# Kernel optimization log

Measured on AMD Instinct MI355X. Metric: run time of the kernel, lower is better.

## Reference

```python
import jax, jax.numpy as jnp
import numpy as np

B, S, D_MODEL, N_HEAD, D_HEAD, GROUPS = 2, 1024, 768, 12, 64, 4
EPS = 1e-9
SCALE = 1.0 / np.sqrt(D_HEAD).astype(np.float32)


def grouped_proj(x, W, b=None):
    # grouped 1x1 Conv1d == block-diagonal linear. x: [B,S,D], W: [g, D/g, O/g]
    g = W.shape[0]
    b_, s_, d = x.shape
    y = jnp.einsum("bsgi,gio->bsgo", x.reshape(b_, s_, g, d // g), W).reshape(b_, s_, -1)
    return y if b is None else y + b


def rel_shift_gather(pos_attn, context_len, shift):
    # HF Funnel _relative_shift_gather
    b, n, s, m = pos_attn.shape
    pos_attn = pos_attn.reshape(b, n, m, s)[:, :, shift:, :]
    pos_attn = pos_attn.reshape(b, n, s, m - shift)[..., :context_len]
    return pos_attn


def setup_inputs() -> dict:
    key = jax.random.key(0)
    ks = jax.random.split(key, 16)
    dg = D_MODEL // GROUPS          # in-channels per group
    og = (N_HEAD * D_HEAD) // GROUPS  # out-channels per group
    std = 0.02
    return {
        "query": jax.random.normal(ks[0], (B, S, D_MODEL), jnp.float32),
        "position_embeds": jax.random.normal(ks[1], (2 * S - 1, D_MODEL), jnp.float32),
        "Wq": jax.random.normal(ks[2], (GROUPS, dg, og), jnp.float32) * std,
        "Wk": jax.random.normal(ks[3], (GROUPS, dg, og), jnp.float32) * std,
        "bk": jnp.zeros((N_HEAD * D_HEAD,), jnp.float32),
        "Wv": jax.random.normal(ks[4], (GROUPS, dg, dg), jnp.float32) * std,
        "bv": jnp.zeros((D_MODEL,), jnp.float32),
        "r_kernel": jax.random.normal(ks[5], (D_MODEL, N_HEAD, D_HEAD), jnp.float32) * std,
        "r_w_bias": jax.random.normal(ks[6], (N_HEAD, D_HEAD), jnp.float32) * std,
        "r_r_bias": jax.random.normal(ks[7], (N_HEAD, D_HEAD), jnp.float32) * std,
        "Wo": jax.random.normal(ks[8], (D_MODEL, D_MODEL), jnp.float32) * std,
        "bo": jnp.zeros((D_MODEL,), jnp.float32),
        "gamma": jnp.ones((D_MODEL,), jnp.float32),
        "beta": jnp.zeros((D_MODEL,), jnp.float32),
    }


def reference(query, position_embeds, Wq, Wk, bk, Wv, bv, r_kernel, r_w_bias,
              r_r_bias, Wo, bo, gamma, beta):
    b, s, _ = query.shape
    # q/k/v via grouped 1x1 convs
    q = grouped_proj(query, Wq).reshape(b, s, N_HEAD, D_HEAD) * SCALE
    k = grouped_proj(query, Wk, bk).reshape(b, s, N_HEAD, D_HEAD)
    v = grouped_proj(query, Wv, bv).reshape(b, s, N_HEAD, D_MODEL // N_HEAD)
    # content stream: (q + u) k^T
    content_score = jnp.einsum("bind,bjnd->bnij", q + r_w_bias * SCALE, k)
    # position stream: (q + v) r^T over 2S-1 relative positions, then rel-shift
    r_head = jnp.einsum("td,dnh->tnh", position_embeds, r_kernel)
    pos_score = jnp.einsum("bind,tnd->bnit", q + r_r_bias * SCALE, r_head)
    pos_score = rel_shift_gather(pos_score, s, shift=1)
    attn_prob = jax.nn.softmax(content_score + pos_score, axis=-1)
    attn_vec = jnp.einsum("bnij,bjnd->bind", attn_prob, v).reshape(b, s, D_MODEL)
    attn_out = attn_vec @ Wo + bo
    # residual + layer norm (eps=1e-9)
    h = query + attn_out
    mu = jnp.mean(h, axis=-1, keepdims=True)
    var = jnp.mean(jnp.square(h - mu), axis=-1, keepdims=True)
    return (h - mu) * jax.lax.rsqrt(var + EPS) * gamma + beta
```

## Files before the change

### kernel.cpp

```cpp
#include <hip/hip_runtime.h>
#include <stdint.h>

#define B_ 2
#define S_ 1024
#define D_ 768
#define H_ 12
#define DH 64
#define G_ 4
#define DG 192
#define T_ 2047
#define SCALEF 0.125f

typedef unsigned short u16;
typedef unsigned int u32;
typedef __attribute__((ext_vector_type(8))) short short8;
typedef __attribute__((ext_vector_type(4))) float floatx4;

__device__ __forceinline__ float uas(u32 x){ union { u32 i; float f; } v; v.i = x; return v.f; }
__device__ __forceinline__ float bf2f(u16 u){ return uas(((u32)u) << 16); }
__device__ __forceinline__ u16 f2bf(float f){
    union { float f; u32 i; } v; v.f = f;
    u32 x = v.i;
    u32 r = (x + 0x7fffu + ((x >> 16) & 1u)) >> 16;
    return (u16)r;
}
__device__ __forceinline__ short8 cvt8(float4 x, float4 y){
    union { u16 h[8]; short8 v; } u;
    u.h[0]=f2bf(x.x); u.h[1]=f2bf(x.y); u.h[2]=f2bf(x.z); u.h[3]=f2bf(x.w);
    u.h[4]=f2bf(y.x); u.h[5]=f2bf(y.y); u.h[6]=f2bf(y.z); u.h[7]=f2bf(y.w);
    return u.v;
}

__global__ __launch_bounds__(256) void pre_kernel(
    const float* __restrict__ query,
    const float* __restrict__ Wq, const float* __restrict__ Wk, const float* __restrict__ Wv,
    const float* __restrict__ bk, const float* __restrict__ bv,
    u16* __restrict__ qq, u16* __restrict__ ko, u16* __restrict__ vt,
    const float* __restrict__ pe, const float* __restrict__ rk,
    u16* __restrict__ R)
{
    __shared__ __align__(16) char sm[49664];
    int tid  = threadIdx.x;
    int wave = tid >> 6, lane = tid & 63;
    int qm   = lane & 15;
    int quad = lane >> 4;
    int id = blockIdx.x;
    int sn = tid & 31, sk = tid >> 5;

    if (id < 768) {
        typedef u16 (*W3T)[32][200];
        W3T Ws = (W3T)sm;
        int m0 = (id & 31) * 64;
        int gy = id >> 5;
        int g  = gy / 6;
        int n0 = (gy % 6) * 32;
        const float* Wm[3] = { Wq, Wk, Wv };

        int row = m0 + wave*16 + qm;
        const float* Ab = query + (size_t)row*D_ + g*DG;
        float4 fx[6], fy[6];
        #pragma unroll
        for (int kc = 0; kc < 6; kc++) {
            fx[kc] = *(const float4*)(Ab + kc*32 + quad*8);
            fy[kc] = *(const float4*)(Ab + kc*32 + quad*8 + 4);
        }
        #pragma unroll
        for (int md = 0; md < 3; md++) {
            const float* W = Wm[md] + (size_t)g*DG*DG + n0 + sn;
            #pragma unroll
            for (int k = 0; k < 24; k++)
                Ws[md][sn][sk + k*8] = f2bf(W[(size_t)(sk + k*8)*DG]);
        }
        __syncthreads();

        short8 af[6];
        #pragma unroll
        for (int kc = 0; kc < 6; kc++) af[kc] = cvt8(fx[kc], fy[kc]);

        floatx4 acc[3][2];
        #pragma unroll
        for (int md = 0; md < 3; md++) { acc[md][0] = (floatx4){0,0,0,0}; acc[md][1] = (floatx4){0,0,0,0}; }
        #pragma unroll
        for (int kc = 0; kc < 6; kc++) {
            short8 a = af[kc];
            #pragma unroll
            for (int md = 0; md < 3; md++) {
                #pragma unroll
                for (int bt = 0; bt < 2; bt++) {
                    short8 b = *(const short8*)&Ws[md][bt*16 + qm][kc*32 + quad*8];
                    acc[md][bt] = __builtin_amdgcn_mfma_f32_16x16x32_bf16(a, b, acc[md][bt], 0,0,0);
                }
            }
        }

        int rowbase = m0 + wave*16 + quad*4;
        int b  = rowbase >> 10;
        int s0 = rowbase & 1023;
        #pragma unroll
        for (int bt = 0; bt < 2; bt++) {
            int c = g*DG + n0 + bt*16 + qm;
            int n = c >> 6, d = c & 63;
            int bn = b*H_ + n;
            float bkv = bk[c], bvv = bv[c];
            #pragma unroll
            for (int gg = 0; gg < 4; gg++) {
                size_t o = ((size_t)bn*S_ + s0 + gg)*DH + d;
                qq[o] = f2bf(acc[0][bt][gg]*SCALEF);
                ko[o] = f2bf(acc[1][bt][gg] + bkv);
            }
            union { u16 h[4]; uint2 v; } vv;
            #pragma unroll
            for (int gg = 0; gg < 4; gg++) vv.h[gg] = f2bf(acc[2][bt][gg] + bvv);
            *(uint2*)(vt + ((size_t)bn*DH + d)*S_ + s0) = vv.v;
        }
    } else {
        typedef u16 (*WsT)[776];
        WsT Ws = (WsT)sm;
        int id2 = id - 768;
        int m0 = (id2 & 31) * 64;
        int n0 = (id2 >> 5) * 32;

        int row = m0 + wave*16 + qm;
        int rowc = (row <= 2046) ? row : 2046;
        const float* Ab = pe + (size_t)rowc*D_;

        float4 fr[4][2];
        #pragma unroll
        for (int t = 0; t < 4; t++) {
            fr[t][0] = *(const float4*)(Ab + t*32 + quad*8);
            fr[t][1] = *(const float4*)(Ab + t*32 + quad*8 + 4);
        }
        {
            const float* W = rk + n0 + sn;
            #pragma unroll
            for (int k = 0; k < 96; k++)
                Ws[sn][sk + k*8] = f2bf(W[(size_t)(sk + k*8)*D_]);
        }
        __syncthreads();

        floatx4 acc[2];
        acc[0] = (floatx4){0,0,0,0};
        acc[1] = (floatx4){0,0,0,0};
        #pragma unroll
        for (int kc = 0; kc < 24; kc++) {
            float4 x = fr[kc & 3][0], y = fr[kc & 3][1];
            if (kc < 20) {
                fr[kc & 3][0] = *(const float4*)(Ab + (kc+4)*32 + quad*8);
                fr[kc & 3][1] = *(const float4*)(Ab + (kc+4)*32 + quad*8 + 4);
            }
            short8 a = cvt8(x, y);
            #pragma unroll
            for (int bt = 0; bt < 2; bt++) {
                short8 b = *(const short8*)&Ws[bt*16 + qm][kc*32 + quad*8];
                acc[bt] = __builtin_amdgcn_mfma_f32_16x16x32_bf16(a, b, acc[bt], 0,0,0);
            }
        }

        #pragma unroll
        for (int bt = 0; bt < 2; bt++) {
            int c = n0 + bt*16 + qm;
            #pragma unroll
            for (int g = 0; g < 4; g++) {
                int r2 = m0 + wave*16 + quad*4 + g;
                if (r2 < T_)
                    R[((size_t)(c >> 6)*T_ + r2)*DH + (c & 63)] = f2bf(acc[bt][g]);
            }
        }
    }
}

__global__ __launch_bounds__(256) void gemm_out_kernel(
    const u16* __restrict__ A, const float* __restrict__ W,
    const float* __restrict__ bias, const float* __restrict__ resid,
    float* __restrict__ outf)
{
    __shared__ __align__(16) u16 Ws[32][776];
    int tid  = threadIdx.x;
    int wave = tid >> 6, lane = tid & 63;
    int qm   = lane & 15;
    int quad = lane >> 4;
    int id = blockIdx.x;
    int m0 = (id & 31) * 64;
    int n0 = (id >> 5) * 32;
    int sn = tid & 31, sk = tid >> 5;

    int row = m0 + wave*16 + qm;
    const u16* Ab = A + (size_t)row*D_;

    short8 ar[8];
    #pragma unroll
    for (int t = 0; t < 8; t++) ar[t] = *(const short8*)(Ab + t*32 + quad*8);
    {
        const float* Wb = W + n0 + sn;
        #pragma unroll
        for (int k = 0; k < 96; k++)
            Ws[sn][sk + k*8] = f2bf(Wb[(size_t)(sk + k*8)*D_]);
    }
    __syncthreads();

    floatx4 acc[2];
    acc[0] = (floatx4){0,0,0,0};
    acc[1] = (floatx4){0,0,0,0};
    #pragma unroll
    for (int kc = 0; kc < 24; kc++) {
        short8 a = ar[kc & 7];
        if (kc < 16) ar[kc & 7] = *(const short8*)(Ab + (kc+8)*32 + quad*8);
        #pragma unroll
        for (int bt = 0; bt < 2; bt++) {
            short8 b = *(const short8*)&Ws[bt*16 + qm][kc*32 + quad*8];
            acc[bt] = __builtin_amdgcn_mfma_f32_16x16x32_bf16(a, b, acc[bt], 0,0,0);
        }
    }

    #pragma unroll
    for (int bt = 0; bt < 2; bt++) {
        int c = n0 + bt*16 + qm;
        #pragma unroll
        for (int g = 0; g < 4; g++) {
            int r2 = m0 + wave*16 + quad*4 + g;
            outf[(size_t)r2*D_ + c] = acc[bt][g] + bias[c] + resid[(size_t)r2*D_ + c];
        }
    }
}

__global__ __launch_bounds__(256, 2) void attn_kernel(
    const u16* __restrict__ qq,
    const u16* __restrict__ kk, const u16* __restrict__ vt,
    const u16* __restrict__ R,
    const float* __restrict__ rwb, const float* __restrict__ rrb,
    u16* __restrict__ av)
{
    __shared__ char smem[64*1024];
    u16* SC  = (u16*)smem;
    u16* PSC = (u16*)(smem + 32768);
    int tid  = threadIdx.x;
    int wave = tid >> 6, lane = tid & 63;
    int qm   = lane & 15;
    int quad = lane >> 4;
    int k8   = quad * 8;
    int blkid = blockIdx.x;
    int xcd = blkid & 7;
    int sl  = blkid >> 3;
    int it  = sl & 63;
    int seg = sl >> 6;
    int bn  = xcd + 8*seg;
    int b = bn / H_, n = bn % H_;
    int i0 = it * 16;
    size_t hbase = (size_t)bn * S_ * DH;

    short8 qcf[2], qpf[2];
    #pragma unroll
    for (int s = 0; s < 2; s++) {
        const u16* qptr = qq + hbase + (size_t)(i0 + qm)*DH + s*32 + k8;
        const float* rwp = rwb + n*DH + s*32 + k8;
        const float* rrp = rrb + n*DH + s*32 + k8;
        #pragma unroll
        for (int j = 0; j < 8; j++) {
            float qv = bf2f(qptr[j]);
            qcf[s][j] = (short)f2bf(qv + rwp[j]*SCALEF);
            qpf[s][j] = (short)f2bf(qv + rrp[j]*SCALEF);
        }
    }

    {
        const u16* kbb = kk + hbase + (size_t)qm*DH + k8;
        short8 rb[8][2];
        #pragma unroll
        for (int t = 0; t < 8; t++) {
            const u16* kp = kbb + (size_t)((wave*16 + t)*16)*DH;
            rb[t][0] = *(const short8*)(kp);
            rb[t][1] = *(const short8*)(kp + 32);
        }
        #pragma unroll
        for (int t = 0; t < 16; t++) {
            short8 b0 = rb[t & 7][0], b1 = rb[t & 7][1];
            if (t < 8) {
                const u16* kp = kbb + (size_t)((wave*16 + t + 8)*16)*DH;
                rb[t & 7][0] = *(const short8*)(kp);
                rb[t & 7][1] = *(const short8*)(kp + 32);
            }
            floatx4 acc = {0.f,0.f,0.f,0.f};
            acc = __builtin_amdgcn_mfma_f32_16x16x32_bf16(qcf[0], b0, acc, 0,0,0);
            acc = __builtin_amdgcn_mfma_f32_16x16x32_bf16(qcf[1], b1, acc, 0,0,0);
            int j0 = (wave*16 + t) * 16;
            #pragma unroll
            for (int g = 0; g < 4; g++)
                SC[(quad*4 + g)*1024 + j0 + qm] = f2bf(acc[g]);
        }
    }

    int ubase = 1008 - i0;
    {
        const u16* rbb = R + (size_t)n*T_*DH + k8;
        short8 rb[8][2];
        int us[8];
        #pragma unroll
        for (int t = 0; t < 8; t++) {
            int m = t*4 + wave;
            int uu = ubase + m*16 + qm;
            int ur = (uu <= 2046) ? uu : 2046;
            us[t] = uu;
            const u16* rp = rbb + (size_t)ur*DH;
            rb[t][0] = *(const short8*)(rp);
            rb[t][1] = *(const short8*)(rp + 32);
        }
        #pragma unroll
        for (int t = 0; t < 16; t++) {
            short8 b0 = rb[t & 7][0], b1 = rb[t & 7][1];
            int uu = us[t & 7];
            if (t < 8) {
                int m2 = (t + 8)*4 + wave;
                int uu2 = ubase + m2*16 + qm;
                int ur2 = (uu2 <= 2046) ? uu2 : 2046;
                us[t & 7] = uu2;
                const u16* rp = rbb + (size_t)ur2*DH;
                rb[t & 7][0] = *(const short8*)(rp);
                rb[t & 7][1] = *(const short8*)(rp + 32);
            }
            floatx4 acc = {0.f,0.f,0.f,0.f};
            acc = __builtin_amdgcn_mfma_f32_16x16x32_bf16(qpf[0], b0, acc, 0,0,0);
            acc = __builtin_amdgcn_mfma_f32_16x16x32_bf16(qpf[1], b1, acc, 0,0,0);
            #pragma unroll
            for (int g = 0; g < 4; g++) {
                int row = quad*4 + g;
                int j = uu + i0 + row - 1024;
                if (j >= 0 && j < S_ && uu <= 2046)
                    PSC[row*1024 + j] = f2bf(acc[g]);
            }
        }
    }
    if (wave == 0) {
        int uu = ubase + 64*16 + qm;
        int ur = (uu <= 2046) ? uu : 2046;
        const u16* rp = R + ((size_t)n*T_ + ur)*DH + k8;
        short8 b0 = *(const short8*)(rp);
        short8 b1 = *(const short8*)(rp + 32);
        floatx4 acc = {0.f,0.f,0.f,0.f};
        acc = __builtin_amdgcn_mfma_f32_16x16x32_bf16(qpf[0], b0, acc, 0,0,0);
        acc = __builtin_amdgcn_mfma_f32_16x16x32_bf16(qpf[1], b1, acc, 0,0,0);
        #pragma unroll
        for (int g = 0; g < 4; g++) {
            int row = quad*4 + g;
            int j = uu + i0 + row - 1024;
            if (j >= 0 && j < S_ && uu <= 2046)
                PSC[row*1024 + j] = f2bf(acc[g]);
        }
    }
    if (i0 == 0 && tid == 0) {
        float sdot = 0.f;
        const u16* r0p = R + (size_t)n*T_*DH;
        const u16* q1p = qq + hbase + DH;
        for (int d = 0; d < DH; d++)
            sdot += (bf2f(q1p[d]) + rrb[n*DH + d]*SCALEF) * bf2f(r0p[d]);
        PSC[1023] = f2bf(sdot);
    }
    __syncthreads();

    for (int rr = 0; rr < 4; rr++) {
        int r = wave*4 + rr;
        short8 c0 = *(const short8*)(SC  + r*1024 + lane*16);
        short8 c1 = *(const short8*)(SC  + r*1024 + lane*16 + 8);
        short8 p0 = *(const short8*)(PSC + r*1024 + lane*16);
        short8 p1 = *(const short8*)(PSC + r*1024 + lane*16 + 8);
        float p[16];
        float mx = -1e30f;
        #pragma unroll
        for (int q = 0; q < 8; q++) {
            p[q]   = bf2f((u16)c0[q]) + bf2f((u16)p0[q]);
            p[q+8] = bf2f((u16)c1[q]) + bf2f((u16)p1[q]);
        }
        #pragma unroll
        for (int q = 0; q < 16; q++) mx = fmaxf(mx, p[q]);
        #pragma unroll
        for (int off = 32; off; off >>= 1) mx = fmaxf(mx, __shfl_xor(mx, off));
        float ssum = 0.f;
        #pragma unroll
        for (int q = 0; q < 16; q++) { p[q] = __expf(p[q] - mx); ssum += p[q]; }
        #pragma unroll
        for (int off = 32; off; off >>= 1) ssum += __shfl_xor(ssum, off);
        float inv = 1.0f / ssum;
        int swz = r & 7;
        union { u16 h[8]; short8 v; } w0, w1;
        #pragma unroll
        for (int q = 0; q < 8; q++) {
            w0.h[q] = f2bf(p[q]*inv);
            w1.h[q] = f2bf(p[q+8]*inv);
        }
        *(short8*)(SC + r*1024 + (((2*lane)   ^ swz) << 3)) = w0.v;
        *(short8*)(SC + r*1024 + (((2*lane+1) ^ swz) << 3)) = w1.v;
    }

    int d0 = wave*16;
    const u16* vbase = vt + ((size_t)bn*DH + d0 + qm)*S_;
    short8 vb[8];
    #pragma unroll
    for (int t = 0; t < 8; t++) vb[t] = *(const short8*)(vbase + t*32 + k8);
    __syncthreads();

    floatx4 o[4];
    #pragma unroll
    for (int t = 0; t < 4; t++) o[t] = (floatx4){0.f,0.f,0.f,0.f};
    int aswz = qm & 7;
    #pragma unroll
    for (int kt = 0; kt < 32; kt++) {
        short8 bfr = vb[kt & 7];
        if (kt < 24) vb[kt & 7] = *(const short8*)(vbase + (kt + 8)*32 + k8);
        int chunk = (kt*4 + quad) ^ aswz;
        short8 a = *(const short8*)(SC + qm*1024 + (chunk << 3));
        o[kt & 3] = __builtin_amdgcn_mfma_f32_16x16x32_bf16(a, bfr, o[kt & 3], 0,0,0);
    }
    floatx4 os = (o[0] + o[1]) + (o[2] + o[3]);
    #pragma unroll
    for (int g = 0; g < 4; g++) {
        int row = quad*4 + g;
        av[((size_t)(b*S_) + i0 + row)*D_ + n*DH + d0 + qm] = f2bf(os[g]);
    }
}

__global__ __launch_bounds__(256) void ln_kernel(
    const float* __restrict__ gamma, const float* __restrict__ beta,
    float* out)
{
    __shared__ float hb[8][D_];
    int tid = threadIdx.x;
    int rowg0 = blockIdx.x * 8;
    #pragma unroll
    for (int p = 0; p < 6; p++) {
        int id = p*256 + tid;
        int r = id / 192, e4 = id % 192;
        *(float4*)&hb[r][e4*4] = *(const float4*)&out[(size_t)(rowg0 + r)*D_ + e4*4];
    }
    __syncthreads();
    int wave = tid >> 6, lane = tid & 63;
    for (int rr = 0; rr < 2; rr++) {
        int r = wave*2 + rr;
        float s = 0.f;
        #pragma unroll
        for (int kq = 0; kq < 12; kq++) s += hb[r][lane + kq*64];
        #pragma unroll
        for (int off = 32; off; off >>= 1) s += __shfl_xor(s, off);
        float mu = s * (1.0f/768.0f);
        float vsum = 0.f;
        #pragma unroll
        for (int kq = 0; kq < 12; kq++) { float d = hb[r][lane + kq*64] - mu; vsum += d*d; }
        #pragma unroll
        for (int off = 32; off; off >>= 1) vsum += __shfl_xor(vsum, off);
        float rstd = rsqrtf(vsum * (1.0f/768.0f) + 1e-9f);
        #pragma unroll
        for (int kq = 0; kq < 3; kq++) {
            int c4 = lane + kq*64;
            float4 g4 = *(const float4*)&gamma[c4*4];
            float4 b4 = *(const float4*)&beta[c4*4];
            float4 h4 = *(const float4*)&hb[r][c4*4];
            float4 o4;
            o4.x = (h4.x - mu)*rstd*g4.x + b4.x;
            o4.y = (h4.y - mu)*rstd*g4.y + b4.y;
            o4.z = (h4.z - mu)*rstd*g4.z + b4.z;
            o4.w = (h4.w - mu)*rstd*g4.w + b4.w;
            *(float4*)&out[(size_t)(rowg0 + r)*D_ + c4*4] = o4;
        }
    }
}

extern "C" void kernel_launch(void* const* d_in, const int* in_sizes, int n_in,
                              void* d_out, int out_size, void* d_ws, size_t ws_size,
                              hipStream_t stream) {
    const float* query = (const float*)d_in[0];
    const float* pe    = (const float*)d_in[1];
    const float* Wq    = (const float*)d_in[2];
    const float* Wk    = (const float*)d_in[3];
    const float* bk    = (const float*)d_in[4];
    const float* Wv    = (const float*)d_in[5];
    const float* bv    = (const float*)d_in[6];
    const float* rk    = (const float*)d_in[7];
    const float* rwb   = (const float*)d_in[8];
    const float* rrb   = (const float*)d_in[9];
    const float* Wo    = (const float*)d_in[10];
    const float* bo    = (const float*)d_in[11];
    const float* gamma = (const float*)d_in[12];
    const float* beta  = (const float*)d_in[13];
    float* out = (float*)d_out;

    u16* ws = (u16*)d_ws;
    const size_t SEG = (size_t)B_*H_*S_*DH;
    u16* qq = ws;
    u16* kk = qq + SEG;
    u16* vt = kk + SEG;
    u16* R  = vt + SEG;
    u16* av = R + SEG;

    pre_kernel<<<1536, 256, 0, stream>>>(query, Wq, Wk, Wv, bk, bv, qq, kk, vt, pe, rk, R);
    attn_kernel<<<1536, 256, 0, stream>>>(qq, kk, vt, R, rwb, rrb, av);
    gemm_out_kernel<<<768, 256, 0, stream>>>(av, Wo, bo, query, out);
    ln_kernel<<<256, 256, 0, stream>>>(gamma, beta, out);
}
```

Baseline: 212.3 us.

## Store K, V and R in MFMA fragment-ready layouts for coalesced attention loads

```diff
diff --git a/kernel.cpp b/kernel.cpp
--- a/kernel.cpp
+++ b/kernel.cpp
@@ -31,13 +31,14 @@
     return u.v;
 }
 
+
 __global__ __launch_bounds__(256) void pre_kernel(
     const float* __restrict__ query,
     const float* __restrict__ Wq, const float* __restrict__ Wk, const float* __restrict__ Wv,
     const float* __restrict__ bk, const float* __restrict__ bv,
-    u16* __restrict__ qq, u16* __restrict__ ko, u16* __restrict__ vt,
+    u16* __restrict__ qq, u16* __restrict__ kf, u16* __restrict__ vf,
     const float* __restrict__ pe, const float* __restrict__ rk,
-    u16* __restrict__ R)
+    u16* __restrict__ Rf)
 {
     __shared__ __align__(16) char sm[49664];
     int tid  = threadIdx.x;
@@ -101,17 +102,19 @@
             int c = g*DG + n0 + bt*16 + qm;
             int n = c >> 6, d = c & 63;
             int bn = b*H_ + n;
+            int p  = d >> 5, dd = d & 31;
+            int qv = (dd >> 3) * 16, jj = dd & 7;
+            int ds = d >> 4, qmv = d & 15;
             float bkv = bk[c], bvv = bv[c];
             #pragma unroll
             for (int gg = 0; gg < 4; gg++) {
-                size_t o = ((size_t)bn*S_ + s0 + gg)*DH + d;
-                qq[o] = f2bf(acc[0][bt][gg]*SCALEF);
-                ko[o] = f2bf(acc[1][bt][gg] + bkv);
-            }
-            union { u16 h[4]; uint2 v; } vv;
-            #pragma unroll
-            for (int gg = 0; gg < 4; gg++) vv.h[gg] = f2bf(acc[2][bt][gg] + bvv);
-            *(uint2*)(vt + ((size_t)bn*DH + d)*S_ + s0) = vv.v;
+                int s = s0 + gg;
+                qq[((size_t)bn*S_ + s)*DH + d] = f2bf(acc[0][bt][gg]*SCALEF);
+                kf[((size_t)bn*64 + (s>>4))*1024 + p*512 + (qv + (s&15))*8 + jj]
+                    = f2bf(acc[1][bt][gg] + bkv);
+                vf[(((size_t)bn*32 + (s>>5))*4 + ds)*512 + (((s>>3)&3)*16 + qmv)*8 + (s&7)]
+                    = f2bf(acc[2][bt][gg] + bvv);
+            }
         }
     } else {
         typedef u16 (*WsT)[776];
@@ -159,11 +162,15 @@
         #pragma unroll
         for (int bt = 0; bt < 2; bt++) {
             int c = n0 + bt*16 + qm;
+            int n = c >> 6, d = c & 63;
+            int p = d >> 5, dd = d & 31;
+            int qv = (dd >> 3) * 16, jj = dd & 7;
             #pragma unroll
             for (int g = 0; g < 4; g++) {
-                int r2 = m0 + wave*16 + quad*4 + g;
-                if (r2 < T_)
-                    R[((size_t)(c >> 6)*T_ + r2)*DH + (c & 63)] = f2bf(acc[bt][g]);
+                int t = m0 + wave*16 + quad*4 + g;
+                if (t < T_)
+                    Rf[((size_t)n*128 + (t>>4))*1024 + p*512 + (qv + (t&15))*8 + jj]
+                        = f2bf(acc[bt][g]);
             }
         }
     }
@@ -225,8 +232,8 @@
 
 __global__ __launch_bounds__(256, 2) void attn_kernel(
     const u16* __restrict__ qq,
-    const u16* __restrict__ kk, const u16* __restrict__ vt,
-    const u16* __restrict__ R,
+    const u16* __restrict__ kf, const u16* __restrict__ vf,
+    const u16* __restrict__ Rf,
     const float* __restrict__ rwb, const float* __restrict__ rrb,
     u16* __restrict__ av)
 {
@@ -263,21 +270,19 @@
     }
 
     {
-        const u16* kbb = kk + hbase + (size_t)qm*DH + k8;
+        const u16* kbb = kf + ((size_t)bn*64 + wave*16)*1024 + lane*8;
         short8 rb[8][2];
         #pragma unroll
         for (int t = 0; t < 8; t++) {
-            const u16* kp = kbb + (size_t)((wave*16 + t)*16)*DH;
-            rb[t][0] = *(const short8*)(kp);
-            rb[t][1] = *(const short8*)(kp + 32);
+            rb[t][0] = *(const short8*)(kbb + t*1024);
+            rb[t][1] = *(const short8*)(kbb + t*1024 + 512);
         }
         #pragma unroll
         for (int t = 0; t < 16; t++) {
             short8 b0 = rb[t & 7][0], b1 = rb[t & 7][1];
             if (t < 8) {
-                const u16* kp = kbb + (size_t)((wave*16 + t + 8)*16)*DH;
-                rb[t & 7][0] = *(const short8*)(kp);
-                rb[t & 7][1] = *(const short8*)(kp + 32);
+                rb[t & 7][0] = *(const short8*)(kbb + (t+8)*1024);
+                rb[t & 7][1] = *(const short8*)(kbb + (t+8)*1024 + 512);
             }
             floatx4 acc = {0.f,0.f,0.f,0.f};
             acc = __builtin_amdgcn_mfma_f32_16x16x32_bf16(qcf[0], b0, acc, 0,0,0);
@@ -289,33 +294,24 @@
         }
     }
 
-    int ubase = 1008 - i0;
     {
-        const u16* rbb = R + (size_t)n*T_*DH + k8;
+        const u16* rbb = Rf + (size_t)n*131072 + lane*8;
+        int ut0 = 63 - it;
         short8 rb[8][2];
-        int us[8];
         #pragma unroll
         for (int t = 0; t < 8; t++) {
-            int m = t*4 + wave;
-            int uu = ubase + m*16 + qm;
-            int ur = (uu <= 2046) ? uu : 2046;
-            us[t] = uu;
-            const u16* rp = rbb + (size_t)ur*DH;
-            rb[t][0] = *(const short8*)(rp);
-            rb[t][1] = *(const short8*)(rp + 32);
+            int ut = ut0 + t*4 + wave;
+            rb[t][0] = *(const short8*)(rbb + (size_t)ut*1024);
+            rb[t][1] = *(const short8*)(rbb + (size_t)ut*1024 + 512);
         }
         #pragma unroll
         for (int t = 0; t < 16; t++) {
             short8 b0 = rb[t & 7][0], b1 = rb[t & 7][1];
-            int uu = us[t & 7];
+            int uu = (ut0 + t*4 + wave)*16 + qm;
             if (t < 8) {
-                int m2 = (t + 8)*4 + wave;
-                int uu2 = ubase + m2*16 + qm;
-                int ur2 = (uu2 <= 2046) ? uu2 : 2046;
-                us[t & 7] = uu2;
-                const u16* rp = rbb + (size_t)ur2*DH;
-                rb[t & 7][0] = *(const short8*)(rp);
-                rb[t & 7][1] = *(const short8*)(rp + 32);
+                int ut2 = ut0 + (t+8)*4 + wave;
+                rb[t & 7][0] = *(const short8*)(rbb + (size_t)ut2*1024);
+                rb[t & 7][1] = *(const short8*)(rbb + (size_t)ut2*1024 + 512);
             }
             floatx4 acc = {0.f,0.f,0.f,0.f};
             acc = __builtin_amdgcn_mfma_f32_16x16x32_bf16(qpf[0], b0, acc, 0,0,0);
@@ -330,11 +326,11 @@
         }
     }
     if (wave == 0) {
-        int uu = ubase + 64*16 + qm;
-        int ur = (uu <= 2046) ? uu : 2046;
-        const u16* rp = R + ((size_t)n*T_ + ur)*DH + k8;
+        int ut = 127 - it;
+        const u16* rp = Rf + (size_t)n*131072 + (size_t)ut*1024 + lane*8;
         short8 b0 = *(const short8*)(rp);
-        short8 b1 = *(const short8*)(rp + 32);
+        short8 b1 = *(const short8*)(rp + 512);
+        int uu = ut*16 + qm;
         floatx4 acc = {0.f,0.f,0.f,0.f};
         acc = __builtin_amdgcn_mfma_f32_16x16x32_bf16(qpf[0], b0, acc, 0,0,0);
         acc = __builtin_amdgcn_mfma_f32_16x16x32_bf16(qpf[1], b1, acc, 0,0,0);
@@ -348,10 +344,12 @@
     }
     if (i0 == 0 && tid == 0) {
         float sdot = 0.f;
-        const u16* r0p = R + (size_t)n*T_*DH;
         const u16* q1p = qq + hbase + DH;
-        for (int d = 0; d < DH; d++)
-            sdot += (bf2f(q1p[d]) + rrb[n*DH + d]*SCALEF) * bf2f(r0p[d]);
+        for (int d = 0; d < DH; d++) {
+            int p = d >> 5, dd = d & 31;
+            u16 rv = Rf[(size_t)n*131072 + p*512 + ((dd>>3)*16 + 0)*8 + (dd&7)];
+            sdot += (bf2f(q1p[d]) + rrb[n*DH + d]*SCALEF) * bf2f(rv);
+        }
         PSC[1023] = f2bf(sdot);
     }
     __syncthreads();
@@ -390,11 +388,10 @@
         *(short8*)(SC + r*1024 + (((2*lane+1) ^ swz) << 3)) = w1.v;
     }
 
-    int d0 = wave*16;
-    const u16* vbase = vt + ((size_t)bn*DH + d0 + qm)*S_;
+    const u16* vbase = vf + (size_t)bn*65536 + wave*512 + lane*8;
     short8 vb[8];
     #pragma unroll
-    for (int t = 0; t < 8; t++) vb[t] = *(const short8*)(vbase + t*32 + k8);
+    for (int t = 0; t < 8; t++) vb[t] = *(const short8*)(vbase + t*2048);
     __syncthreads();
 
     floatx4 o[4];
@@ -404,12 +401,13 @@
     #pragma unroll
     for (int kt = 0; kt < 32; kt++) {
         short8 bfr = vb[kt & 7];
-        if (kt < 24) vb[kt & 7] = *(const short8*)(vbase + (kt + 8)*32 + k8);
+        if (kt < 24) vb[kt & 7] = *(const short8*)(vbase + (size_t)(kt+8)*2048);
         int chunk = (kt*4 + quad) ^ aswz;
         short8 a = *(const short8*)(SC + qm*1024 + (chunk << 3));
         o[kt & 3] = __builtin_amdgcn_mfma_f32_16x16x32_bf16(a, bfr, o[kt & 3], 0,0,0);
     }
     floatx4 os = (o[0] + o[1]) + (o[2] + o[3]);
+    int d0 = wave*16;
     #pragma unroll
     for (int g = 0; g < 4; g++) {
         int row = quad*4 + g;
@@ -484,13 +482,13 @@
     u16* ws = (u16*)d_ws;
     const size_t SEG = (size_t)B_*H_*S_*DH;
     u16* qq = ws;
-    u16* kk = qq + SEG;
-    u16* vt = kk + SEG;
-    u16* R  = vt + SEG;
-    u16* av = R + SEG;
-
-    pre_kernel<<<1536, 256, 0, stream>>>(query, Wq, Wk, Wv, bk, bv, qq, kk, vt, pe, rk, R);
-    attn_kernel<<<1536, 256, 0, stream>>>(qq, kk, vt, R, rwb, rrb, av);
+    u16* kf = qq + SEG;
+    u16* vf = kf + SEG;
+    u16* Rf = vf + SEG;
+    u16* av = Rf + SEG;
+
+    pre_kernel<<<1536, 256, 0, stream>>>(query, Wq, Wk, Wv, bk, bv, qq, kf, vf, pe, rk, Rf);
+    attn_kernel<<<1536, 256, 0, stream>>>(qq, kf, vf, Rf, rwb, rrb, av);
     gemm_out_kernel<<<768, 256, 0, stream>>>(av, Wo, bo, query, out);
     ln_kernel<<<256, 256, 0, stream>>>(gamma, beta, out);
 }
```

Result: faster. 177.7 us (-16.3%).
